# Optimization experiments

Hardware: AMD Instinct MI355X
Metric: run time of the kernel (lower is better)

Reference implementation:

```python
import jax, jax.numpy as jnp
import numpy as np

N_NODES = 4096
N_EDGES = 16384
F_IN = 64
F_EDGE = 16
HID = 128
OUT = 64
N_GRAPHS = 32


def _encoder(x, edge_index, edge_attr, batch, p):
    N = x.shape[0]
    src, dst = edge_index[0], edge_index[1]
    # EdgeMLP: [E, F_edge] -> [E, F_in * HID] per-edge weight matrices
    h = jax.nn.relu(edge_attr @ p['e_w1'] + p['e_b1'])
    h = jax.nn.relu(h @ p['e_w2'] + p['e_b2'])
    Wmat = (h @ p['e_w3'] + p['e_b3']).reshape(-1, x.shape[1], p['root_w'].shape[1])  # [E, F_in, HID]
    # NNConv: message = x_src @ W_edge, scatter-add to dst, plus root transform + bias
    msg = jnp.einsum('ei,eio->eo', x[src], Wmat)  # [E, HID]
    agg = jax.ops.segment_sum(msg, dst, num_segments=N)
    h1 = jax.nn.relu(agg + x @ p['root_w'] + p['conv1_b'])  # [N, HID]
    # GATConv (1 head, concat=False) with self-loops (PyG default)
    loop = jnp.arange(N, dtype=src.dtype)
    si = jnp.concatenate([src, loop])
    di = jnp.concatenate([dst, loop])
    hp = h1 @ p['gat_w']  # [N, HID]
    a_s = hp @ p['att_src']  # [N]
    a_d = hp @ p['att_dst']  # [N]
    e = jax.nn.leaky_relu(a_s[si] + a_d[di], negative_slope=0.2)
    m = jax.ops.segment_max(e, di, num_segments=N)
    ex = jnp.exp(e - m[di])
    denom = jax.ops.segment_sum(ex, di, num_segments=N)
    alpha = ex / (denom[di] + 1e-16)
    h2 = jax.ops.segment_sum(alpha[:, None] * hp[si], di, num_segments=N) + p['gat_b']
    h2 = jax.nn.relu(h2)
    # global mean pool over graphs
    s = jax.ops.segment_sum(h2, batch, num_segments=N_GRAPHS)
    cnt = jax.ops.segment_sum(jnp.ones((N,), h2.dtype), batch, num_segments=N_GRAPHS)
    pooled = s / jnp.maximum(cnt, 1.0)[:, None]
    return jax.nn.relu(pooled @ p['fc1_w'] + p['fc1_b'])  # [B, OUT]


def setup_inputs() -> dict:
    key = jax.random.key(0)
    ks = jax.random.split(key, 24)
    d = {}
    d['x1'] = jax.random.normal(ks[0], (N_NODES, F_IN), jnp.float32)
    d['edge_index1'] = jax.random.randint(ks[1], (2, N_EDGES), 0, N_NODES)
    d['edge_attr1'] = jax.random.normal(ks[2], (N_EDGES, F_EDGE), jnp.float32)
    d['batch1'] = jnp.sort(jax.random.randint(ks[3], (N_NODES,), 0, N_GRAPHS))
    d['x2'] = jax.random.normal(ks[4], (N_NODES, F_IN), jnp.float32)
    d['edge_index2'] = jax.random.randint(ks[5], (2, N_EDGES), 0, N_NODES)
    d['edge_attr2'] = jax.random.normal(ks[6], (N_EDGES, F_EDGE), jnp.float32)
    d['batch2'] = jnp.sort(jax.random.randint(ks[7], (N_NODES,), 0, N_GRAPHS))

    def lin(k, fi, fo):
        return jax.random.normal(k, (fi, fo), jnp.float32) * (fi ** -0.5)

    d['e_w1'] = lin(ks[8], F_EDGE, 128); d['e_b1'] = jnp.zeros((128,), jnp.float32)
    d['e_w2'] = lin(ks[9], 128, 64); d['e_b2'] = jnp.zeros((64,), jnp.float32)
    d['e_w3'] = lin(ks[10], 64, F_IN * HID); d['e_b3'] = jnp.zeros((F_IN * HID,), jnp.float32)
    d['root_w'] = lin(ks[11], F_IN, HID); d['conv1_b'] = jnp.zeros((HID,), jnp.float32)
    d['gat_w'] = lin(ks[12], HID, HID)
    d['att_src'] = jax.random.normal(ks[13], (HID,), jnp.float32) * (HID ** -0.5)
    d['att_dst'] = jax.random.normal(ks[14], (HID,), jnp.float32) * (HID ** -0.5)
    d['gat_b'] = jnp.zeros((HID,), jnp.float32)
    d['fc1_w'] = lin(ks[15], HID, OUT); d['fc1_b'] = jnp.zeros((OUT,), jnp.float32)
    d['fc2_w'] = lin(ks[16], OUT, 1); d['fc2_b'] = jnp.zeros((1,), jnp.float32)
    return d


def reference(x1, edge_index1, edge_attr1, batch1, x2, edge_index2, edge_attr2, batch2,
              e_w1, e_b1, e_w2, e_b2, e_w3, e_b3, root_w, conv1_b,
              gat_w, att_src, att_dst, gat_b, fc1_w, fc1_b, fc2_w, fc2_b):
    p = dict(e_w1=e_w1, e_b1=e_b1, e_w2=e_w2, e_b2=e_b2, e_w3=e_w3, e_b3=e_b3,
             root_w=root_w, conv1_b=conv1_b, gat_w=gat_w, att_src=att_src,
             att_dst=att_dst, gat_b=gat_b, fc1_w=fc1_w, fc1_b=fc1_b,
             fc2_w=fc2_w, fc2_b=fc2_b)
    z1 = _encoder(x1, edge_index1, edge_attr1, batch1, p)
    z2 = _encoder(x2, edge_index2, edge_attr2, batch2, p)
    z = jnp.abs(z1 - z2) @ fc2_w + fc2_b  # [B, 1]
    return jax.nn.sigmoid(z).squeeze(1)  # [B]
```

## Files before the change

### kernel.cpp

```cpp
#include <hip/hip_runtime.h>
#include <hip/hip_bf16.h>
#include <math.h>

#define NN 4096
#define NE 16384
#define FIN 64
#define FE 16
#define HIDD 128
#define OUTD 64
#define NG 32
#define EP (NE + NN)
#define KSPLIT 4
#define NCH (64 / KSPLIT)

typedef __attribute__((ext_vector_type(4))) unsigned u4v;
typedef __attribute__((ext_vector_type(4))) float f4v;
typedef _Float16 f16x8 __attribute__((ext_vector_type(8)));

union FragH { u4v u; f16x8 h; };
union FH2 { _Float16 f[2]; unsigned u; };

__global__ void k_splitB(const float* __restrict__ w3, unsigned short* __restrict__ B1t) {
    __shared__ float lds[64 * 129];
    int c = blockIdx.x, t = threadIdx.x;
#pragma unroll
    for (int r = 0; r < 32; ++r) {
        int idx = r * 256 + t;
        lds[(idx >> 7) * 129 + (idx & 127)] = w3[(size_t)c * 8192 + idx];
    }
    __syncthreads();
#pragma unroll
    for (int r = 0; r < 32; ++r) {
        int e = r * 256 + t;
        float v = lds[(e & 63) * 129 + (e >> 6)];
        union { _Float16 f; unsigned short u; } cv;
        cv.f = (_Float16)v;
        B1t[(size_t)c * 8192 + e] = cv.u;
    }
}

#define PB_EMLP  4096
#define PB_BIAS  (PB_EMLP + 4096)
#define PB_TOTAL (PB_BIAS + 32)

__global__ void k_prep(const float* __restrict__ ea0, const float* __restrict__ ea1,
                       const float* __restrict__ w1, const float* __restrict__ b1,
                       const float* __restrict__ w2, const float* __restrict__ b2,
                       const float* __restrict__ X0, const float* __restrict__ X1,
                       const float* __restrict__ b3,
                       const int* __restrict__ ei0, const int* __restrict__ ei1,
                       float* __restrict__ h0, float* __restrict__ h1g,
                       float* __restrict__ Bb0, float* __restrict__ Bb1,
                       int* __restrict__ rowcnt) {
    int b = blockIdx.x, t = threadIdx.x;
    if (b < PB_EMLP) {
        int gi = b >> 11;
        int e0 = (b & 2047) * 8;
        const float* ea = gi ? ea1 : ea0;
        float* hout = gi ? h1g : h0;
        __shared__ float h1s[8][HIDD];
#pragma unroll
        for (int r = 0; r < 4; ++r) {
            int idx = r * 256 + t;
            int e1 = idx >> 7, j = idx & 127;
            float acc = b1[j];
#pragma unroll
            for (int i = 0; i < FE; ++i) acc += ea[(e0 + e1) * FE + i] * w1[i * HIDD + j];
            h1s[e1][j] = fmaxf(acc, 0.f);
        }
        __syncthreads();
#pragma unroll
        for (int r = 0; r < 2; ++r) {
            int idx = r * 256 + t;
            int e1 = idx >> 6, j = idx & 63;
            float acc = b2[j];
#pragma unroll 16
            for (int k = 0; k < HIDD; ++k) acc += h1s[e1][k] * w2[k * 64 + j];
            hout[(size_t)(e0 + e1) * 64 + j] = fmaxf(acc, 0.f);
        }
    } else if (b < PB_BIAS) {
        int bb = b - PB_EMLP;
        int gi = bb >> 11;
        int n = (bb & 2047) * 2 + (t >> 7);
        int o = t & 127;
        const float* X = gi ? X1 : X0;
        float* Bb = gi ? Bb1 : Bb0;
        float acc = 0.f;
#pragma unroll 16
        for (int i = 0; i < FIN; ++i) acc += X[n * FIN + i] * b3[i * HIDD + o];
        Bb[(size_t)n * HIDD + o] = acc;
    } else {
        int tid = (b - PB_BIAS) * 256 + t;
        for (int idx = tid; idx < 2 * EP; idx += 32 * 256) {
            int gi = idx / EP, e = idx % EP;
            const int* dst = (gi ? ei1 : ei0) + NE;
            int d = (e < NE) ? dst[e] : e - NE;
            atomicAdd(&rowcnt[gi * NN + d], 1);
        }
    }
}

__global__ void k_scan(const int* __restrict__ rowcnt, int* __restrict__ rowptr,
                       const int* __restrict__ batch0, const int* __restrict__ batch1,
                       int* __restrict__ br) {
    int b = blockIdx.x;
    if (b < 2) {
        int gi = b;
        const int* cnt = rowcnt + gi * NN;
        int* rp = rowptr + gi * (NN + 1);
        int t = threadIdx.x;
        int base = t * 4;
        int v0 = cnt[base], v1 = cnt[base + 1], v2 = cnt[base + 2], v3 = cnt[base + 3];
        int s = v0 + v1 + v2 + v3;
        __shared__ int sc[1024];
        sc[t] = s;
        __syncthreads();
        for (int off = 1; off < 1024; off <<= 1) {
            int a = (t >= off) ? sc[t - off] : 0;
            __syncthreads();
            sc[t] += a;
            __syncthreads();
        }
        int run = sc[t] - s;
        rp[base] = run; run += v0;
        rp[base + 1] = run; run += v1;
        rp[base + 2] = run; run += v2;
        rp[base + 3] = run; run += v3;
        if (t == 1023) rp[NN] = run;
    } else {
        int t = threadIdx.x;
        if (t < 66) {
            int gi = t / 33, g = t % 33;
            const int* batch = gi ? batch1 : batch0;
            int lo = 0, hi = NN;
            while (lo < hi) {
                int mid = (lo + hi) >> 1;
                if (batch[mid] < g) lo = mid + 1; else hi = mid;
            }
            br[gi * 33 + g] = lo;
        }
    }
}

__global__ void k_fill(const int* __restrict__ ei0, const int* __restrict__ ei1,
                       const int* __restrict__ rowptr, int* __restrict__ cnt2,
                       int* __restrict__ adj) {
    int idx = blockIdx.x * 256 + threadIdx.x;
    if (idx >= 2 * EP) return;
    int gi = idx / EP, e = idx % EP;
    const int* dst = (gi ? ei1 : ei0) + NE;
    int d = (e < NE) ? dst[e] : e - NE;
    int pos = rowptr[gi * (NN + 1) + d] + atomicAdd(&cnt2[gi * NN + d], 1);
    adj[gi * EP + pos] = e;
}

__global__ void __launch_bounds__(128, 2)
k_nnconv(const float* __restrict__ x0, const float* __restrict__ x1,
         const float* __restrict__ h_0, const float* __restrict__ h_1,
         const unsigned short* __restrict__ B1t,
         const float* __restrict__ Bb0, const float* __restrict__ Bb1,
         const int* __restrict__ ei0, const int* __restrict__ ei1,
         float* __restrict__ msg) {
    __shared__ __align__(16) float sm[32 * 128];
    int gi = blockIdx.z;
    const float* x = gi ? x1 : x0;
    const float* hh = gi ? h_1 : h_0;
    const float* Bb = gi ? Bb1 : Bb0;
    const int* src = gi ? ei1 : ei0;

    int t = threadIdx.x;
    int e0 = blockIdx.x * 64;
    int z = blockIdx.y;
    int ch = t >> 6;
    int l = t & 63, q4 = l >> 4, c16 = l & 15;

    FragH xf[4][2];
#pragma unroll
    for (int mf = 0; mf < 4; ++mf) {
        int s_ = src[e0 + mf * 16 + c16];
        const float* xr = &x[(size_t)s_ * FIN];
#pragma unroll
        for (int kf = 0; kf < 2; ++kf) {
            float xv[8];
            *(float4*)&xv[0] = *(const float4*)&xr[kf * 32 + q4 * 8];
            *(float4*)&xv[4] = *(const float4*)&xr[kf * 32 + q4 * 8 + 4];
            u4v w;
#pragma unroll
            for (int p = 0; p < 4; ++p) {
                FH2 c2;
                c2.f[0] = (_Float16)xv[2 * p];
                c2.f[1] = (_Float16)xv[2 * p + 1];
                w[p] = c2.u;
            }
            xf[mf][kf].u = w;
        }
    }

    f4v acc[4][4];
#pragma unroll
    for (int a = 0; a < 4; ++a)
#pragma unroll
        for (int b = 0; b < 4; ++b) acc[a][b] = (f4v){0.f, 0.f, 0.f, 0.f};

    const u4v* bp = (const u4v*)B1t;

#define LOADF(buf, cg)                                                          \
    {                                                                           \
        const u4v* cp = bp + (size_t)(cg) * 1024;                               \
        _Pragma("unroll") for (int kf = 0; kf < 2; ++kf)                        \
        _Pragma("unroll") for (int nf = 0; nf < 4; ++nf)                        \
            buf[kf * 4 + nf].u = cp[(ch * 64 + nf * 16 + c16) * 8 + kf * 4 + q4]; \
    }

#define DOMFMA(buf, COMP)                                                       \
    {                                                                           \
        _Pragma("unroll") for (int mf = 0; mf < 4; ++mf) {                      \
            FH2 hp2;                                                            \
            hp2.f[0] = (_Float16)hv4[mf].COMP;                                  \
            hp2.f[1] = hp2.f[0];                                                \
            unsigned hw = hp2.u;                                                \
            FragH hb; hb.u = (u4v){hw, hw, hw, hw};                             \
            _Pragma("unroll") for (int kf = 0; kf < 2; ++kf) {                  \
                FragH a1;                                                       \
                a1.h = hb.h * xf[mf][kf].h;                                     \
                _Pragma("unroll") for (int nf = 0; nf < 4; ++nf) {              \
                    acc[mf][nf] = __builtin_amdgcn_mfma_f32_16x16x32_f16(       \
                        a1.h, buf[kf * 4 + nf].h, acc[mf][nf], 0, 0, 0);        \
                }                                                               \
            }                                                                   \
        }                                                                       \
    }

    FragH bA[8], bB[8];
    float4 hv4[4];
    LOADF(bA, z * NCH);
#pragma unroll 1
    for (int cl = 0; cl < NCH; cl += 4) {
#pragma unroll
        for (int mf = 0; mf < 4; ++mf)
            hv4[mf] = *(const float4*)&hh[(size_t)(e0 + mf * 16 + c16) * 64 + z * NCH + cl];
        LOADF(bB, z * NCH + cl + 1);
        DOMFMA(bA, x);
        LOADF(bA, z * NCH + cl + 2);
        DOMFMA(bB, y);
        LOADF(bB, z * NCH + cl + 3);
        DOMFMA(bA, z);
        if (cl + 4 < NCH) LOADF(bA, z * NCH + cl + 4);
        DOMFMA(bB, w);
    }
#undef LOADF
#undef DOMFMA

    float* mb = msg + (size_t)(gi * KSPLIT + z) * NE * HIDD;
    int z0 = (z == 0);
#pragma unroll
    for (int half = 0; half < 2; ++half) {
        if (half) __syncthreads();
#pragma unroll
        for (int mf2 = 0; mf2 < 2; ++mf2) {
            int mf = half * 2 + mf2;
#pragma unroll
            for (int j = 0; j < 4; ++j) {
                int rr = mf2 * 16 + q4 * 4 + j;
#pragma unroll
                for (int nf = 0; nf < 4; ++nf)
                    sm[rr * 128 + ch * 64 + nf * 16 + c16] = acc[mf][nf][j];
            }
        }
        __syncthreads();
#pragma unroll
        for (int it = 0; it < 8; ++it) {
            int f = it * 128 + t;
            int row = f >> 5, c4 = f & 31;
            int eg = e0 + half * 32 + row;
            float4 v = *(float4*)&sm[row * 128 + c4 * 4];
            if (z0) {
                int s_ = src[eg];
                const float* bbr = &Bb[(size_t)s_ * HIDD + c4 * 4];
                v.x += bbr[0]; v.y += bbr[1]; v.z += bbr[2]; v.w += bbr[3];
            }
            *(float4*)&mb[(size_t)eg * HIDD + c4 * 4] = v;
        }
    }
}

__global__ void k_h1hp(const float* __restrict__ msg,
                       const int* __restrict__ rowptr, const int* __restrict__ adj,
                       const float* __restrict__ X0, const float* __restrict__ X1,
                       const float* __restrict__ rw, const float* __restrict__ cb,
                       const float* __restrict__ gw,
                       const float* __restrict__ asw, const float* __restrict__ adw,
                       float* __restrict__ hp0, float* __restrict__ hp1,
                       float* __restrict__ a_s0, float* __restrict__ a_s1,
                       float* __restrict__ a_d0, float* __restrict__ a_d1) {
    int gi = blockIdx.y;
    const float* X = gi ? X1 : X0;
    float* hp = gi ? hp1 : hp0;
    float* a_s = gi ? a_s1 : a_s0;
    float* a_d = gi ? a_d1 : a_d0;
    const int* rp = rowptr + gi * (NN + 1);
    const int* aj = adj + gi * EP;
    const float* mz0 = msg + (size_t)(gi * KSPLIT + 0) * NE * HIDD;
    const float* mz1 = msg + (size_t)(gi * KSPLIT + 1) * NE * HIDD;
    const float* mz2 = msg + (size_t)(gi * KSPLIT + 2) * NE * HIDD;
    const float* mz3 = msg + (size_t)(gi * KSPLIT + 3) * NE * HIDD;
    int n0 = blockIdx.x * 4;
    int o = threadIdx.x;
    __shared__ float xsh[4][FIN];
    __shared__ float h1s[4][HIDD];
    __shared__ float s1[4][2], s2[4][2];
    xsh[o >> 6][o & 63] = X[n0 * FIN + o];
    xsh[2 + (o >> 6)][o & 63] = X[n0 * FIN + 128 + o];
    __syncthreads();
    float accs[4];
#pragma unroll
    for (int nn = 0; nn < 4; ++nn) {
        int n = n0 + nn;
        float acc = cb[o];
        int lo = rp[n], hi = rp[n + 1];
        for (int p = lo; p < hi; ++p) {
            int e = aj[p];
            if (e < NE) {
                size_t eo = (size_t)e * HIDD + o;
                acc += (mz0[eo] + mz1[eo]) + (mz2[eo] + mz3[eo]);
            }
        }
        accs[nn] = acc;
    }
#pragma unroll 8
    for (int i = 0; i < FIN; ++i) {
        float w = rw[i * HIDD + o];
#pragma unroll
        for (int nn = 0; nn < 4; ++nn) accs[nn] += xsh[nn][i] * w;
    }
#pragma unroll
    for (int nn = 0; nn < 4; ++nn) h1s[nn][o] = fmaxf(accs[nn], 0.f);
    __syncthreads();
#pragma unroll
    for (int nn = 0; nn < 4; ++nn) accs[nn] = 0.f;
#pragma unroll 8
    for (int k = 0; k < HIDD; ++k) {
        float w = gw[k * HIDD + o];
#pragma unroll
        for (int nn = 0; nn < 4; ++nn) accs[nn] += h1s[nn][k] * w;
    }
#pragma unroll
    for (int nn = 0; nn < 4; ++nn) {
        hp[(size_t)(n0 + nn) * HIDD + o] = accs[nn];
        float p1 = accs[nn] * asw[o], p2 = accs[nn] * adw[o];
#pragma unroll
        for (int off = 32; off; off >>= 1) {
            p1 += __shfl_down(p1, off);
            p2 += __shfl_down(p2, off);
        }
        if ((o & 63) == 0) { s1[nn][o >> 6] = p1; s2[nn][o >> 6] = p2; }
    }
    __syncthreads();
    if (o < 4) {
        a_s[n0 + o] = s1[o][0] + s1[o][1];
        a_d[n0 + o] = s2[o][0] + s2[o][1];
    }
}

__global__ void k_gat(const int* __restrict__ rowptr, const int* __restrict__ adj,
                      const int* __restrict__ ei0, const int* __restrict__ ei1,
                      const float* __restrict__ hp0, const float* __restrict__ hp1,
                      const float* __restrict__ as0, const float* __restrict__ as1,
                      const float* __restrict__ ad0, const float* __restrict__ ad1,
                      const float* __restrict__ gb,
                      float* __restrict__ h2_0, float* __restrict__ h2_1) {
    int gi = blockIdx.y;
    const int* src = gi ? ei1 : ei0;
    const float* hp = gi ? hp1 : hp0;
    const float* a_s = gi ? as1 : as0;
    const float* a_d = gi ? ad1 : ad0;
    float* h2 = gi ? h2_1 : h2_0;
    const int* rp = rowptr + gi * (NN + 1);
    const int* aj = adj + gi * EP;
    int w = threadIdx.x >> 6, l = threadIdx.x & 63;
    int n = blockIdx.x * 4 + w;
    int lo = rp[n], deg = rp[n + 1] - lo;
    float adn = a_d[n];
    float m = -1e30f;
    for (int base = 0; base < deg; base += 64) {
        float sc = -1e30f;
        int j = base + l;
        if (j < deg) {
            int e = aj[lo + j];
            int si = (e < NE) ? src[e] : n;
            float xsc = a_s[si] + adn;
            sc = xsc > 0.f ? xsc : 0.2f * xsc;
        }
#pragma unroll
        for (int off = 32; off; off >>= 1) sc = fmaxf(sc, __shfl_xor(sc, off));
        m = fmaxf(m, sc);
    }
    float den = 0.f;
    for (int base = 0; base < deg; base += 64) {
        float ev = 0.f;
        int j = base + l;
        if (j < deg) {
            int e = aj[lo + j];
            int si = (e < NE) ? src[e] : n;
            float xsc = a_s[si] + adn;
            float sc = xsc > 0.f ? xsc : 0.2f * xsc;
            ev = expf(sc - m);
        }
#pragma unroll
        for (int off = 32; off; off >>= 1) ev += __shfl_xor(ev, off);
        den += ev;
    }
    float inv = 1.f / (den + 1e-16f);
    float acc0 = 0.f, acc1 = 0.f;
    for (int j = 0; j < deg; ++j) {
        int e = aj[lo + j];
        int si = (e < NE) ? src[e] : n;
        float xsc = a_s[si] + adn;
        float sc = xsc > 0.f ? xsc : 0.2f * xsc;
        float al = expf(sc - m) * inv;
        acc0 += al * hp[(size_t)si * HIDD + l];
        acc1 += al * hp[(size_t)si * HIDD + 64 + l];
    }
    h2[(size_t)n * HIDD + l] = fmaxf(acc0 + gb[l], 0.f);
    h2[(size_t)n * HIDD + 64 + l] = fmaxf(acc1 + gb[64 + l], 0.f);
}

__global__ void k_poolfc1(const float* __restrict__ h2_0, const float* __restrict__ h2_1,
                          const int* __restrict__ br,
                          const float* __restrict__ w, const float* __restrict__ bias,
                          float* __restrict__ z) {
    int gi = blockIdx.x >> 5, g = blockIdx.x & 31;
    const float* h2 = gi ? h2_1 : h2_0;
    int lo = br[gi * 33 + g], hi = br[gi * 33 + g + 1];
    int t = threadIdx.x;
    __shared__ float pool[HIDD];
    float acc = 0.f;
    for (int n = lo; n < hi; ++n) acc += h2[(size_t)n * HIDD + t];
    pool[t] = acc;
    __syncthreads();
    if (t < 64) {
        float c = fmaxf((float)(hi - lo), 1.f);
        float a = bias[t];
#pragma unroll 16
        for (int o = 0; o < HIDD; ++o) a += (pool[o] / c) * w[o * OUTD + t];
        z[gi * NG * OUTD + g * OUTD + t] = fmaxf(a, 0.f);
    }
}

__global__ void k_final(const float* __restrict__ zz,
                        const float* __restrict__ w, const float* __restrict__ b,
                        float* __restrict__ out) {
    int g = threadIdx.x;
    const float* z1 = zz;
    const float* z2 = zz + NG * OUTD;
    float acc = b[0];
#pragma unroll
    for (int j = 0; j < OUTD; ++j) acc += fabsf(z1[g * OUTD + j] - z2[g * OUTD + j]) * w[j];
    out[g] = 1.f / (1.f + expf(-acc));
}

extern "C" void kernel_launch(void* const* d_in, const int* in_sizes, int n_in,
                              void* d_out, int out_size, void* d_ws, size_t ws_size,
                              hipStream_t stream) {
    const float* x0     = (const float*)d_in[0];
    const int*   ei0    = (const int*)d_in[1];
    const float* ea0    = (const float*)d_in[2];
    const int*   b0     = (const int*)d_in[3];
    const float* x1     = (const float*)d_in[4];
    const int*   ei1    = (const int*)d_in[5];
    const float* ea1    = (const float*)d_in[6];
    const int*   b1     = (const int*)d_in[7];
    const float* e_w1 = (const float*)d_in[8];
    const float* e_b1 = (const float*)d_in[9];
    const float* e_w2 = (const float*)d_in[10];
    const float* e_b2 = (const float*)d_in[11];
    const float* e_w3 = (const float*)d_in[12];
    const float* e_b3 = (const float*)d_in[13];
    const float* root_w = (const float*)d_in[14];
    const float* conv1_b = (const float*)d_in[15];
    const float* gat_w = (const float*)d_in[16];
    const float* att_src = (const float*)d_in[17];
    const float* att_dst = (const float*)d_in[18];
    const float* gat_b = (const float*)d_in[19];
    const float* fc1_w = (const float*)d_in[20];
    const float* fc1_b = (const float*)d_in[21];
    const float* fc2_w = (const float*)d_in[22];
    const float* fc2_b = (const float*)d_in[23];

    float* ws = (float*)d_ws;
    size_t off = 0;
    auto alloc = [&](size_t n) { float* p = ws + off; off += n; return p; };
    int* rowcnt = (int*)alloc(2 * NN);
    int* cnt2   = (int*)alloc(2 * NN);
    size_t zero_elems = off;
    int* rowptr = (int*)alloc(2 * (NN + 1));
    int* br     = (int*)alloc(66);
    int* adj    = (int*)alloc(2 * EP);
    float* h[2]   = {alloc((size_t)NE * 64), alloc((size_t)NE * 64)};
    unsigned short* B1t = (unsigned short*)alloc((size_t)4096 * 128 / 2);
    float* Bb[2]  = {alloc((size_t)NN * HIDD), alloc((size_t)NN * HIDD)};
    float* msg    = alloc((size_t)2 * KSPLIT * NE * HIDD);
    float* hp[2]  = {alloc((size_t)NN * HIDD), alloc((size_t)NN * HIDD)};
    float* a_s[2] = {alloc(NN), alloc(NN)};
    float* a_d[2] = {alloc(NN), alloc(NN)};
    float* h2[2]  = {alloc((size_t)NN * HIDD), alloc((size_t)NN * HIDD)};
    float* zz     = alloc((size_t)2 * NG * OUTD);

    (void)hipMemsetAsync(ws, 0, zero_elems * 4, stream);
    k_splitB<<<64, 256, 0, stream>>>(e_w3, B1t);
    k_prep<<<PB_TOTAL, 256, 0, stream>>>(ea0, ea1, e_w1, e_b1, e_w2, e_b2,
                                         x0, x1, e_b3, ei0, ei1,
                                         h[0], h[1], Bb[0], Bb[1],
                                         rowcnt);
    k_scan<<<3, 1024, 0, stream>>>(rowcnt, rowptr, b0, b1, br);
    k_fill<<<(2 * EP + 255) / 256, 256, 0, stream>>>(ei0, ei1, rowptr, cnt2, adj);
    k_nnconv<<<dim3(NE / 64, KSPLIT, 2), 128, 0, stream>>>(
        x0, x1, h[0], h[1], B1t, Bb[0], Bb[1], ei0, ei1, msg);
    k_h1hp<<<dim3(NN / 4, 2), HIDD, 0, stream>>>(
        msg, rowptr, adj, x0, x1, root_w, conv1_b, gat_w, att_src, att_dst,
        hp[0], hp[1], a_s[0], a_s[1], a_d[0], a_d[1]);
    k_gat<<<dim3(NN / 4, 2), 256, 0, stream>>>(
        rowptr, adj, ei0, ei1, hp[0], hp[1], a_s[0], a_s[1], a_d[0], a_d[1],
        gat_b, h2[0], h2[1]);
    k_poolfc1<<<64, HIDD, 0, stream>>>(h2[0], h2[1], br, fc1_w, fc1_b, zz);
    k_final<<<1, NG, 0, stream>>>(zz, fc2_w, fc2_b, (float*)d_out);
}
```

Measured before the change: 249.4 us.

## Store NNConv partial messages in fp16 with fewer K-splits; widen h1hp blocks

The NNConv kernel now writes its per-edge partial messages as fp16 instead of fp32, and the K-split drops from 4 to 2. This cuts the size of the intermediate msg buffer written by k_nnconv and read back by k_h1hp several-fold. k_h1hp now handles 16 nodes per 512-thread block instead of 4 per 128-thread block. In exchange, messages lose precision to fp16 rounding, and each nnconv block does twice the K work with half as many blocks.

```diff
diff --git a/kernel.cpp b/kernel.cpp
--- a/kernel.cpp
+++ b/kernel.cpp
@@ -10,7 +10,7 @@
 #define OUTD 64
 #define NG 32
 #define EP (NE + NN)
-#define KSPLIT 4
+#define KSPLIT 2
 #define NCH (64 / KSPLIT)
 
 typedef __attribute__((ext_vector_type(4))) unsigned u4v;
@@ -19,6 +19,7 @@
 
 union FragH { u4v u; f16x8 h; };
 union FH2 { _Float16 f[2]; unsigned u; };
+union F16x8U { _Float16 f[8]; u4v u; };
 
 __global__ void k_splitB(const float* __restrict__ w3, unsigned short* __restrict__ B1t) {
     __shared__ float lds[64 * 129];
@@ -160,7 +161,7 @@
          const unsigned short* __restrict__ B1t,
          const float* __restrict__ Bb0, const float* __restrict__ Bb1,
          const int* __restrict__ ei0, const int* __restrict__ ei1,
-         float* __restrict__ msg) {
+         _Float16* __restrict__ msgh) {
     __shared__ __align__(16) float sm[32 * 128];
     int gi = blockIdx.z;
     const float* x = gi ? x1 : x0;
@@ -251,7 +252,7 @@
 #undef LOADF
 #undef DOMFMA
 
-    float* mb = msg + (size_t)(gi * KSPLIT + z) * NE * HIDD;
+    _Float16* mb = msgh + (size_t)(gi * KSPLIT + z) * NE * HIDD;
     int z0 = (z == 0);
 #pragma unroll
     for (int half = 0; half < 2; ++half) {
@@ -269,22 +270,28 @@
         }
         __syncthreads();
 #pragma unroll
-        for (int it = 0; it < 8; ++it) {
-            int f = it * 128 + t;
-            int row = f >> 5, c4 = f & 31;
+        for (int it = 0; it < 4; ++it) {
+            int u = it * 128 + t;
+            int row = u >> 4, c8 = u & 15;
             int eg = e0 + half * 32 + row;
-            float4 v = *(float4*)&sm[row * 128 + c4 * 4];
+            float v[8];
+            *(float4*)&v[0] = *(float4*)&sm[row * 128 + c8 * 8];
+            *(float4*)&v[4] = *(float4*)&sm[row * 128 + c8 * 8 + 4];
             if (z0) {
                 int s_ = src[eg];
-                const float* bbr = &Bb[(size_t)s_ * HIDD + c4 * 4];
-                v.x += bbr[0]; v.y += bbr[1]; v.z += bbr[2]; v.w += bbr[3];
+                const float* bbr = &Bb[(size_t)s_ * HIDD + c8 * 8];
+#pragma unroll
+                for (int j = 0; j < 8; ++j) v[j] += bbr[j];
             }
-            *(float4*)&mb[(size_t)eg * HIDD + c4 * 4] = v;
-        }
-    }
-}
-
-__global__ void k_h1hp(const float* __restrict__ msg,
+            F16x8U cv;
+#pragma unroll
+            for (int j = 0; j < 8; ++j) cv.f[j] = (_Float16)v[j];
+            *(u4v*)&mb[(size_t)eg * HIDD + c8 * 8] = cv.u;
+        }
+    }
+}
+
+__global__ void k_h1hp(const _Float16* __restrict__ msgh,
                        const int* __restrict__ rowptr, const int* __restrict__ adj,
                        const float* __restrict__ X0, const float* __restrict__ X1,
                        const float* __restrict__ rw, const float* __restrict__ cb,
@@ -300,29 +307,31 @@
     float* a_d = gi ? a_d1 : a_d0;
     const int* rp = rowptr + gi * (NN + 1);
     const int* aj = adj + gi * EP;
-    const float* mz0 = msg + (size_t)(gi * KSPLIT + 0) * NE * HIDD;
-    const float* mz1 = msg + (size_t)(gi * KSPLIT + 1) * NE * HIDD;
-    const float* mz2 = msg + (size_t)(gi * KSPLIT + 2) * NE * HIDD;
-    const float* mz3 = msg + (size_t)(gi * KSPLIT + 3) * NE * HIDD;
-    int n0 = blockIdx.x * 4;
-    int o = threadIdx.x;
-    __shared__ float xsh[4][FIN];
-    __shared__ float h1s[4][HIDD];
-    __shared__ float s1[4][2], s2[4][2];
-    xsh[o >> 6][o & 63] = X[n0 * FIN + o];
-    xsh[2 + (o >> 6)][o & 63] = X[n0 * FIN + 128 + o];
+    const _Float16* m0 = msgh + (size_t)(gi * KSPLIT + 0) * NE * HIDD;
+    const _Float16* m1 = msgh + (size_t)(gi * KSPLIT + 1) * NE * HIDD;
+    int n0 = blockIdx.x * 16;
+    int t = threadIdx.x;
+    int o = t & 127, q = t >> 7;
+    __shared__ float xsh[16][FIN];
+    __shared__ float h1s[16][HIDD];
+    __shared__ float s1[16][2], s2[16][2];
+#pragma unroll
+    for (int r = 0; r < 2; ++r) {
+        int idx = r * 512 + t;
+        xsh[idx >> 6][idx & 63] = X[(n0 + (idx >> 6)) * FIN + (idx & 63)];
+    }
     __syncthreads();
     float accs[4];
 #pragma unroll
     for (int nn = 0; nn < 4; ++nn) {
-        int n = n0 + nn;
+        int n = n0 + q * 4 + nn;
         float acc = cb[o];
         int lo = rp[n], hi = rp[n + 1];
         for (int p = lo; p < hi; ++p) {
             int e = aj[p];
             if (e < NE) {
                 size_t eo = (size_t)e * HIDD + o;
-                acc += (mz0[eo] + mz1[eo]) + (mz2[eo] + mz3[eo]);
+                acc += (float)m0[eo] + (float)m1[eo];
             }
         }
         accs[nn] = acc;
@@ -331,10 +340,10 @@
     for (int i = 0; i < FIN; ++i) {
         float w = rw[i * HIDD + o];
 #pragma unroll
-        for (int nn = 0; nn < 4; ++nn) accs[nn] += xsh[nn][i] * w;
-    }
-#pragma unroll
-    for (int nn = 0; nn < 4; ++nn) h1s[nn][o] = fmaxf(accs[nn], 0.f);
+        for (int nn = 0; nn < 4; ++nn) accs[nn] += xsh[q * 4 + nn][i] * w;
+    }
+#pragma unroll
+    for (int nn = 0; nn < 4; ++nn) h1s[q * 4 + nn][o] = fmaxf(accs[nn], 0.f);
     __syncthreads();
 #pragma unroll
     for (int nn = 0; nn < 4; ++nn) accs[nn] = 0.f;
@@ -342,23 +351,24 @@
     for (int k = 0; k < HIDD; ++k) {
         float w = gw[k * HIDD + o];
 #pragma unroll
-        for (int nn = 0; nn < 4; ++nn) accs[nn] += h1s[nn][k] * w;
+        for (int nn = 0; nn < 4; ++nn) accs[nn] += h1s[q * 4 + nn][k] * w;
     }
 #pragma unroll
     for (int nn = 0; nn < 4; ++nn) {
-        hp[(size_t)(n0 + nn) * HIDD + o] = accs[nn];
+        int n = n0 + q * 4 + nn;
+        hp[(size_t)n * HIDD + o] = accs[nn];
         float p1 = accs[nn] * asw[o], p2 = accs[nn] * adw[o];
 #pragma unroll
         for (int off = 32; off; off >>= 1) {
             p1 += __shfl_down(p1, off);
             p2 += __shfl_down(p2, off);
         }
-        if ((o & 63) == 0) { s1[nn][o >> 6] = p1; s2[nn][o >> 6] = p2; }
+        if ((o & 63) == 0) { s1[q * 4 + nn][o >> 6] = p1; s2[q * 4 + nn][o >> 6] = p2; }
     }
     __syncthreads();
-    if (o < 4) {
-        a_s[n0 + o] = s1[o][0] + s1[o][1];
-        a_d[n0 + o] = s2[o][0] + s2[o][1];
+    if (t < 16) {
+        a_s[n0 + t] = s1[t][0] + s1[t][1];
+        a_d[n0 + t] = s2[t][0] + s2[t][1];
     }
 }
 
@@ -499,7 +509,7 @@
     float* h[2]   = {alloc((size_t)NE * 64), alloc((size_t)NE * 64)};
     unsigned short* B1t = (unsigned short*)alloc((size_t)4096 * 128 / 2);
     float* Bb[2]  = {alloc((size_t)NN * HIDD), alloc((size_t)NN * HIDD)};
-    float* msg    = alloc((size_t)2 * KSPLIT * NE * HIDD);
+    _Float16* msgh = (_Float16*)alloc((size_t)2 * KSPLIT * NE * HIDD / 2);
     float* hp[2]  = {alloc((size_t)NN * HIDD), alloc((size_t)NN * HIDD)};
     float* a_s[2] = {alloc(NN), alloc(NN)};
     float* a_d[2] = {alloc(NN), alloc(NN)};
@@ -515,9 +525,9 @@
     k_scan<<<3, 1024, 0, stream>>>(rowcnt, rowptr, b0, b1, br);
     k_fill<<<(2 * EP + 255) / 256, 256, 0, stream>>>(ei0, ei1, rowptr, cnt2, adj);
     k_nnconv<<<dim3(NE / 64, KSPLIT, 2), 128, 0, stream>>>(
-        x0, x1, h[0], h[1], B1t, Bb[0], Bb[1], ei0, ei1, msg);
-    k_h1hp<<<dim3(NN / 4, 2), HIDD, 0, stream>>>(
-        msg, rowptr, adj, x0, x1, root_w, conv1_b, gat_w, att_src, att_dst,
+        x0, x1, h[0], h[1], B1t, Bb[0], Bb[1], ei0, ei1, msgh);
+    k_h1hp<<<dim3(NN / 16, 2), 512, 0, stream>>>(
+        msgh, rowptr, adj, x0, x1, root_w, conv1_b, gat_w, att_src, att_dst,
         hp[0], hp[1], a_s[0], a_s[1], a_d[0], a_d[1]);
     k_gat<<<dim3(NN / 4, 2), 256, 0, stream>>>(
         rowptr, adj, ei0, ei1, hp[0], hp[1], a_s[0], a_s[1], a_d[0], a_d[1],
```

Measured after the change: 243.0 us. 2.6% less time.
